# Kernel tuning notes

Hardware: AMD Instinct MI355X
Metric: run time of the kernel (lower is better)

## Reference

```python
import jax, jax.numpy as jnp
import numpy as np

DIM = 192
HEADS = 6
WS = 7
N = WS * WS  # 49
B_ = 4096
NW = 64


def _relative_position_index(ws):
    coords = np.stack(np.meshgrid(np.arange(ws), np.arange(ws), indexing='ij'))  # (2, ws, ws)
    cf = coords.reshape(2, -1)  # (2, N)
    rel = cf[:, :, None] - cf[:, None, :]  # (2, N, N)
    rel = rel.transpose(1, 2, 0).copy()
    rel[:, :, 0] += ws - 1
    rel[:, :, 1] += ws - 1
    rel[:, :, 0] *= 2 * ws - 1
    return jnp.asarray(rel.sum(-1), dtype=jnp.int32)  # (N, N)


def setup_inputs() -> dict:
    key = jax.random.key(0)
    ks = jax.random.split(key, 8)
    x = jax.random.normal(ks[0], (B_, N, DIM), dtype=jnp.float32)
    mask = jax.random.normal(ks[1], (NW, N, N), dtype=jnp.float32)
    qkv_w = jax.random.normal(ks[2], (3 * DIM, DIM), dtype=jnp.float32) * 0.02
    qkv_b = jnp.zeros((3 * DIM,), dtype=jnp.float32)
    proj_w = jax.random.normal(ks[3], (DIM, DIM), dtype=jnp.float32) * 0.02
    proj_b = jnp.zeros((DIM,), dtype=jnp.float32)
    n_bias = (2 * WS - 1) * (2 * WS - 1)  # 169
    bias_table = jax.random.truncated_normal(ks[4], -2.0, 2.0, (n_bias, HEADS), dtype=jnp.float32) * 0.02
    rel_idx = _relative_position_index(WS)
    return {"x": x, "mask": mask, "qkv_w": qkv_w, "qkv_b": qkv_b,
            "proj_w": proj_w, "proj_b": proj_b, "bias_table": bias_table,
            "rel_idx": rel_idx}


def reference(x, mask, qkv_w, qkv_b, proj_w, proj_b, bias_table, rel_idx):
    Bw, n, c = x.shape
    hd = c // HEADS
    scale = hd ** -0.5
    qkv = x @ qkv_w.T + qkv_b  # (B_, N, 3C)
    qkv = qkv.reshape(Bw, n, 3, HEADS, hd).transpose(2, 0, 3, 1, 4)  # (3, B_, H, N, hd)
    q, k, v = qkv[0] * scale, qkv[1], qkv[2]
    attn = jnp.einsum('bhqd,bhkd->bhqk', q, k)  # (B_, H, N, N)
    bias = bias_table[rel_idx.reshape(-1)].reshape(n, n, HEADS).transpose(2, 0, 1)  # (H, N, N)
    attn = attn + bias[None]
    nW = mask.shape[0]
    attn = attn.reshape(Bw // nW, nW, HEADS, n, n) + mask[None, :, None]
    attn = jax.nn.softmax(attn.reshape(Bw, HEADS, n, n), axis=-1)
    out = jnp.einsum('bhqk,bhkd->bhqd', attn, v)  # (B_, H, N, hd)
    out = out.transpose(0, 2, 1, 3).reshape(Bw, n, c)
    return out @ proj_w.T + proj_b
```

## Files before the change

### kernel.cpp

```cpp
#include <hip/hip_runtime.h>
#include <hip/hip_fp16.h>


typedef short bf16x8 __attribute__((ext_vector_type(8)));
typedef float f32x4 __attribute__((ext_vector_type(4)));

#define MFMA16(a, b, c) __builtin_amdgcn_mfma_f32_16x16x32_bf16((a), (b), (c), 0, 0, 0)

#define DIMC 192
#define NTOK 49

__device__ __forceinline__ unsigned short f2bf(float f) {
  unsigned int u = __float_as_uint(f);
  u += 0x7fffu + ((u >> 16) & 1u);
  return (unsigned short)(u >> 16);
}

__global__ void prep_kernel(const float* __restrict__ qkv_w,
                            const float* __restrict__ proj_w,
                            const float* __restrict__ bias_table,
                            const int* __restrict__ rel_idx,
                            unsigned short* __restrict__ qkv_wb,
                            unsigned short* __restrict__ proj_wb,
                            float* __restrict__ biasP) {
  int i = blockIdx.x * 256 + threadIdx.x;
  if (i < 576 * 192) qkv_wb[i] = f2bf(qkv_w[i]);
  if (i < 192 * 192) proj_wb[i] = f2bf(proj_w[i]);
  if (i < 6 * 64 * 64) {
    int h = i >> 12;
    int rr = i & 4095;
    int r = rr >> 6, c = rr & 63;
    float v = 0.f;
    if (r < NTOK && c < NTOK) v = bias_table[rel_idx[r * NTOK + c] * 6 + h];
    biasP[i] = v;
  }
}

__global__ __launch_bounds__(256, 2) void winattn_kernel(
    const float* __restrict__ x,
    const float* __restrict__ mask,
    const float* __restrict__ qkv_b,
    const float* __restrict__ proj_b,
    const unsigned short* __restrict__ qkv_wb,
    const unsigned short* __restrict__ proj_wb,
    const float* __restrict__ biasP,
    float* __restrict__ out) {
  __shared__ unsigned short xb[64 * 200];
  __shared__ unsigned short Qs[64 * 40];
  __shared__ unsigned short Ks[64 * 40];
  __shared__ unsigned short Vts[32 * 72];
  __shared__ unsigned short Pb[4 * 16 * 72];
  __shared__ unsigned short Ob[64 * 40];
  __shared__ __half maskS[64 * 64];

  const int tid = threadIdx.x;
  const int b = blockIdx.x;
  const int widx = b & 63;
  const int lane = tid & 63;
  const int wv = tid >> 6;
  const int lq = lane >> 4;
  const int ln = lane & 15;

  {
    const float4* xp = (const float4*)(x + (size_t)b * (NTOK * DIMC));
    for (int i = tid; i < NTOK * DIMC / 4; i += 256) {
      float4 v = xp[i];
      int fl = i * 4;
      int r = fl / DIMC;
      int c = fl - r * DIMC;
      unsigned int lo = (unsigned int)f2bf(v.x) | ((unsigned int)f2bf(v.y) << 16);
      unsigned int hi = (unsigned int)f2bf(v.z) | ((unsigned int)f2bf(v.w) << 16);
      *(uint2*)(&xb[r * 200 + c]) = make_uint2(lo, hi);
    }
    for (int i = tid; i < 15 * 200 / 2; i += 256)
      ((unsigned int*)(&xb[49 * 200]))[i] = 0u;
    const float* mp = mask + (size_t)widx * (NTOK * NTOK);
    for (int i = tid; i < 64 * 64; i += 256) {
      int r = i >> 6, c = i & 63;
      float v = (c >= NTOK) ? -30000.f : ((r >= NTOK) ? 0.f : mp[r * NTOK + c]);
      maskS[i] = __float2half(v);
    }
  }

  f32x4 pacc[4][3];
  for (int nti = 0; nti < 3; ++nti) {
    float pbv = proj_b[(wv * 3 + nti) * 16 + ln];
    for (int mt = 0; mt < 4; ++mt) pacc[mt][nti] = (f32x4){pbv, pbv, pbv, pbv};
  }
  __syncthreads();

  const float scale = 0.17677669529663687f;

  for (int h = 0; h < 6; ++h) {
    for (int tt = 0; tt < 6; tt += 2) {
      int t0 = wv * 6 + tt;
      int t1 = t0 + 1;
      int nt0 = t0 >> 2, mt0 = t0 & 3;
      int nt1 = t1 >> 2, mt1 = t1 & 3;
      int oc0 = (nt0 >> 1) * DIMC + h * 32 + (nt0 & 1) * 16 + ln;
      int oc1 = (nt1 >> 1) * DIMC + h * 32 + (nt1 & 1) * 16 + ln;
      const unsigned short* w0p = qkv_wb + (size_t)oc0 * DIMC + lq * 8;
      const unsigned short* w1p = qkv_wb + (size_t)oc1 * DIMC + lq * 8;
      bf16x8 w0[6], w1[6];
      for (int ks = 0; ks < 6; ++ks) {
        w0[ks] = *(const bf16x8*)(w0p + ks * 32);
        w1[ks] = *(const bf16x8*)(w1p + ks * 32);
      }
      float b0 = qkv_b[oc0], b1 = qkv_b[oc1];
      f32x4 acc0 = (f32x4){b0, b0, b0, b0};
      f32x4 acc1 = (f32x4){b1, b1, b1, b1};
      const unsigned short* a0p = &xb[(mt0 * 16 + ln) * 200 + lq * 8];
      const unsigned short* a1p = &xb[(mt1 * 16 + ln) * 200 + lq * 8];
      for (int ks = 0; ks < 6; ++ks) {
        bf16x8 a0 = *(const bf16x8*)(a0p + ks * 32);
        bf16x8 a1 = *(const bf16x8*)(a1p + ks * 32);
        acc0 = MFMA16(a0, w0[ks], acc0);
        acc1 = MFMA16(a1, w1[ks], acc1);
      }
      {
        int which = nt0 >> 1, db = (nt0 & 1) * 16 + ln, row0 = mt0 * 16 + lq * 4;
        if (which == 0) {
          for (int r = 0; r < 4; ++r) Qs[(row0 + r) * 40 + db] = f2bf(acc0[r] * scale);
        } else if (which == 1) {
          for (int r = 0; r < 4; ++r) Ks[(row0 + r) * 40 + db] = f2bf(acc0[r]);
        } else {
          unsigned int lo = (unsigned int)f2bf(acc0[0]) | ((unsigned int)f2bf(acc0[1]) << 16);
          unsigned int hi = (unsigned int)f2bf(acc0[2]) | ((unsigned int)f2bf(acc0[3]) << 16);
          *(uint2*)(&Vts[db * 72 + row0]) = make_uint2(lo, hi);
        }
      }
      {
        int which = nt1 >> 1, db = (nt1 & 1) * 16 + ln, row0 = mt1 * 16 + lq * 4;
        if (which == 0) {
          for (int r = 0; r < 4; ++r) Qs[(row0 + r) * 40 + db] = f2bf(acc1[r] * scale);
        } else if (which == 1) {
          for (int r = 0; r < 4; ++r) Ks[(row0 + r) * 40 + db] = f2bf(acc1[r]);
        } else {
          unsigned int lo = (unsigned int)f2bf(acc1[0]) | ((unsigned int)f2bf(acc1[1]) << 16);
          unsigned int hi = (unsigned int)f2bf(acc1[2]) | ((unsigned int)f2bf(acc1[3]) << 16);
          *(uint2*)(&Vts[db * 72 + row0]) = make_uint2(lo, hi);
        }
      }
    }
    __syncthreads();

    {
      const int mt = wv;
      bf16x8 kf[4], vf0[2], vf1[2];
      for (int nt = 0; nt < 4; ++nt)
        kf[nt] = *(const bf16x8*)&Ks[(nt * 16 + ln) * 40 + lq * 8];
      for (int nv = 0; nv < 2; ++nv) {
        vf0[nv] = *(const bf16x8*)&Vts[(nv * 16 + ln) * 72 + lq * 8];
        vf1[nv] = *(const bf16x8*)&Vts[(nv * 16 + ln) * 72 + 32 + lq * 8];
      }
      bf16x8 qf = *(const bf16x8*)&Qs[(mt * 16 + ln) * 40 + lq * 8];
      f32x4 sv[4];
      for (int nt = 0; nt < 4; ++nt)
        sv[nt] = MFMA16(qf, kf[nt], ((f32x4){0.f, 0.f, 0.f, 0.f}));

      int row0 = mt * 16 + lq * 4;
      const float* bp = biasP + ((size_t)h * 64 + row0) * 64;
      float tt[4][4];
      for (int nt = 0; nt < 4; ++nt) {
        int col = nt * 16 + ln;
        for (int r = 0; r < 4; ++r)
          tt[nt][r] = sv[nt][r] + bp[r * 64 + col] + __half2float(maskS[(row0 + r) * 64 + col]);
      }
      float pinv[4];
      for (int r = 0; r < 4; ++r) {
        float m = fmaxf(fmaxf(tt[0][r], tt[1][r]), fmaxf(tt[2][r], tt[3][r]));
        m = fmaxf(m, __shfl_xor(m, 1, 64));
        m = fmaxf(m, __shfl_xor(m, 2, 64));
        m = fmaxf(m, __shfl_xor(m, 4, 64));
        m = fmaxf(m, __shfl_xor(m, 8, 64));
        float sum = 0.f;
        for (int nt = 0; nt < 4; ++nt) {
          float e = __expf(tt[nt][r] - m);
          tt[nt][r] = e;
          sum += e;
        }
        sum += __shfl_xor(sum, 1, 64);
        sum += __shfl_xor(sum, 2, 64);
        sum += __shfl_xor(sum, 4, 64);
        sum += __shfl_xor(sum, 8, 64);
        pinv[r] = 1.f / sum;
      }
      unsigned short* Pw = &Pb[wv * 16 * 72];
      for (int nt = 0; nt < 4; ++nt) {
        int col = nt * 16 + ln;
        for (int r = 0; r < 4; ++r) Pw[(lq * 4 + r) * 72 + col] = f2bf(tt[nt][r]);
      }
      bf16x8 pa0 = *(const bf16x8*)&Pw[ln * 72 + lq * 8];
      bf16x8 pa1 = *(const bf16x8*)&Pw[ln * 72 + 32 + lq * 8];
      f32x4 o0 = (f32x4){0.f, 0.f, 0.f, 0.f};
      f32x4 o1 = (f32x4){0.f, 0.f, 0.f, 0.f};
      o0 = MFMA16(pa0, vf0[0], o0);
      o0 = MFMA16(pa1, vf1[0], o0);
      o1 = MFMA16(pa0, vf0[1], o1);
      o1 = MFMA16(pa1, vf1[1], o1);
      for (int r = 0; r < 4; ++r) {
        int row = row0 + r;
        Ob[row * 40 + ln] = f2bf(o0[r] * pinv[r]);
        Ob[row * 40 + 16 + ln] = f2bf(o1[r] * pinv[r]);
      }
    }
    __syncthreads();

    {
      bf16x8 oa[4];
      for (int mt = 0; mt < 4; ++mt)
        oa[mt] = *(const bf16x8*)&Ob[(mt * 16 + ln) * 40 + lq * 8];
      for (int nti = 0; nti < 3; ++nti) {
        int o = (wv * 3 + nti) * 16 + ln;
        bf16x8 w = *(const bf16x8*)(proj_wb + (size_t)o * DIMC + h * 32 + lq * 8);
        for (int mt = 0; mt < 4; ++mt)
          pacc[mt][nti] = MFMA16(oa[mt], w, pacc[mt][nti]);
      }
    }
    __syncthreads();
  }

  {
    float* outp = out + (size_t)b * (NTOK * DIMC);
    for (int nti = 0; nti < 3; ++nti) {
      int col = (wv * 3 + nti) * 16 + ln;
      for (int mt = 0; mt < 4; ++mt) {
        int row0 = mt * 16 + lq * 4;
        for (int r = 0; r < 4; ++r) {
          int row = row0 + r;
          if (row < NTOK) outp[row * DIMC + col] = pacc[mt][nti][r];
        }
      }
    }
  }
}

extern "C" void kernel_launch(void* const* d_in, const int* in_sizes, int n_in,
                              void* d_out, int out_size, void* d_ws, size_t ws_size,
                              hipStream_t stream) {
  const float* x = (const float*)d_in[0];
  const float* mask = (const float*)d_in[1];
  const float* qkv_w = (const float*)d_in[2];
  const float* qkv_b = (const float*)d_in[3];
  const float* proj_w = (const float*)d_in[4];
  const float* proj_b = (const float*)d_in[5];
  const float* bias_table = (const float*)d_in[6];
  const int* rel_idx = (const int*)d_in[7];

  unsigned short* qkv_wb = (unsigned short*)d_ws;
  unsigned short* proj_wb = qkv_wb + 576 * 192;
  float* biasP = (float*)(proj_wb + 192 * 192);

  prep_kernel<<<432, 256, 0, stream>>>(qkv_w, proj_w, bias_table, rel_idx,
                                       qkv_wb, proj_wb, biasP);
  winattn_kernel<<<4096, 256, 0, stream>>>(x, mask, qkv_b, proj_b,
                                           qkv_wb, proj_wb, biasP,
                                           (float*)d_out);
}
```

Before: 611.6 us.

## Alias shared buffers, keep mask in registers, raise occupancy to four blocks

Shared memory drops from about 63KB to about 40KB. The separate buffers become one array with phase-aliased regions: P scratch overlays Q/K, and Ob overlays K/V, made safe by an extra barrier after the fragments are loaded. The per-window mask tile is now loaded directly into registers instead of a half-precision LDS copy. Launch bounds are raised to 4 blocks per CU, and the QKV projection loop is simplified to one tile per iteration with full unrolling. The aim is higher occupancy to hide latency, at the cost of an extra barrier per head and a tighter register budget that may cause spills.

```diff
diff --git a/kernel.cpp b/kernel.cpp
--- a/kernel.cpp
+++ b/kernel.cpp
@@ -36,7 +36,7 @@
   }
 }
 
-__global__ __launch_bounds__(256, 2) void winattn_kernel(
+__global__ __launch_bounds__(256, 4) void winattn_kernel(
     const float* __restrict__ x,
     const float* __restrict__ mask,
     const float* __restrict__ qkv_b,
@@ -45,13 +45,12 @@
     const unsigned short* __restrict__ proj_wb,
     const float* __restrict__ biasP,
     float* __restrict__ out) {
-  __shared__ unsigned short xb[64 * 200];
-  __shared__ unsigned short Qs[64 * 40];
-  __shared__ unsigned short Ks[64 * 40];
-  __shared__ unsigned short Vts[32 * 72];
-  __shared__ unsigned short Pb[4 * 16 * 72];
-  __shared__ unsigned short Ob[64 * 40];
-  __shared__ __half maskS[64 * 64];
+  __shared__ unsigned short smem[20224];
+  unsigned short* xb = smem;
+  unsigned short* Qs = smem + 12800;
+  unsigned short* Ks = smem + 15360;
+  unsigned short* Vts = smem + 17920;
+  unsigned short* Ob = smem + 17408;
 
   const int tid = threadIdx.x;
   const int b = blockIdx.x;
@@ -61,30 +60,43 @@
   const int lq = lane >> 4;
   const int ln = lane & 15;
 
+  unsigned short* Pbw = smem + 12800 + wv * (16 * 72);
+
   {
     const float4* xp = (const float4*)(x + (size_t)b * (NTOK * DIMC));
     for (int i = tid; i < NTOK * DIMC / 4; i += 256) {
       float4 v = xp[i];
-      int fl = i * 4;
-      int r = fl / DIMC;
-      int c = fl - r * DIMC;
+      int r = i / 48;
+      int c = (i - r * 48) * 4;
       unsigned int lo = (unsigned int)f2bf(v.x) | ((unsigned int)f2bf(v.y) << 16);
       unsigned int hi = (unsigned int)f2bf(v.z) | ((unsigned int)f2bf(v.w) << 16);
       *(uint2*)(&xb[r * 200 + c]) = make_uint2(lo, hi);
     }
     for (int i = tid; i < 15 * 200 / 2; i += 256)
       ((unsigned int*)(&xb[49 * 200]))[i] = 0u;
+  }
+
+  const int arow0 = wv * 16 + lq * 4;
+  float mk[4][4];
+  {
     const float* mp = mask + (size_t)widx * (NTOK * NTOK);
-    for (int i = tid; i < 64 * 64; i += 256) {
-      int r = i >> 6, c = i & 63;
-      float v = (c >= NTOK) ? -30000.f : ((r >= NTOK) ? 0.f : mp[r * NTOK + c]);
-      maskS[i] = __float2half(v);
+#pragma unroll
+    for (int nt = 0; nt < 4; ++nt) {
+      int col = nt * 16 + ln;
+#pragma unroll
+      for (int r = 0; r < 4; ++r) {
+        int row = arow0 + r;
+        mk[nt][r] = (col >= NTOK) ? -30000.f
+                                  : ((row >= NTOK) ? 0.f : mp[row * NTOK + col]);
+      }
     }
   }
 
   f32x4 pacc[4][3];
+#pragma unroll
   for (int nti = 0; nti < 3; ++nti) {
     float pbv = proj_b[(wv * 3 + nti) * 16 + ln];
+#pragma unroll
     for (int mt = 0; mt < 4; ++mt) pacc[mt][nti] = (f32x4){pbv, pbv, pbv, pbv};
   }
   __syncthreads();
@@ -92,81 +104,67 @@
   const float scale = 0.17677669529663687f;
 
   for (int h = 0; h < 6; ++h) {
-    for (int tt = 0; tt < 6; tt += 2) {
-      int t0 = wv * 6 + tt;
-      int t1 = t0 + 1;
-      int nt0 = t0 >> 2, mt0 = t0 & 3;
-      int nt1 = t1 >> 2, mt1 = t1 & 3;
-      int oc0 = (nt0 >> 1) * DIMC + h * 32 + (nt0 & 1) * 16 + ln;
-      int oc1 = (nt1 >> 1) * DIMC + h * 32 + (nt1 & 1) * 16 + ln;
-      const unsigned short* w0p = qkv_wb + (size_t)oc0 * DIMC + lq * 8;
-      const unsigned short* w1p = qkv_wb + (size_t)oc1 * DIMC + lq * 8;
-      bf16x8 w0[6], w1[6];
+#pragma unroll
+    for (int t = 0; t < 6; ++t) {
+      int id = wv * 6 + t;
+      int nt = id >> 2, mt = id & 3;
+      int oc = (nt >> 1) * DIMC + h * 32 + (nt & 1) * 16 + ln;
+      const unsigned short* wp = qkv_wb + (size_t)oc * DIMC + lq * 8;
+      bf16x8 w[6];
+#pragma unroll
+      for (int ks = 0; ks < 6; ++ks) w[ks] = *(const bf16x8*)(wp + ks * 32);
+      float b0 = qkv_b[oc];
+      f32x4 acc = (f32x4){b0, b0, b0, b0};
+      const unsigned short* ap = &xb[(mt * 16 + ln) * 200 + lq * 8];
+#pragma unroll
       for (int ks = 0; ks < 6; ++ks) {
-        w0[ks] = *(const bf16x8*)(w0p + ks * 32);
-        w1[ks] = *(const bf16x8*)(w1p + ks * 32);
-      }
-      float b0 = qkv_b[oc0], b1 = qkv_b[oc1];
-      f32x4 acc0 = (f32x4){b0, b0, b0, b0};
-      f32x4 acc1 = (f32x4){b1, b1, b1, b1};
-      const unsigned short* a0p = &xb[(mt0 * 16 + ln) * 200 + lq * 8];
-      const unsigned short* a1p = &xb[(mt1 * 16 + ln) * 200 + lq * 8];
-      for (int ks = 0; ks < 6; ++ks) {
-        bf16x8 a0 = *(const bf16x8*)(a0p + ks * 32);
-        bf16x8 a1 = *(const bf16x8*)(a1p + ks * 32);
-        acc0 = MFMA16(a0, w0[ks], acc0);
-        acc1 = MFMA16(a1, w1[ks], acc1);
-      }
-      {
-        int which = nt0 >> 1, db = (nt0 & 1) * 16 + ln, row0 = mt0 * 16 + lq * 4;
-        if (which == 0) {
-          for (int r = 0; r < 4; ++r) Qs[(row0 + r) * 40 + db] = f2bf(acc0[r] * scale);
-        } else if (which == 1) {
-          for (int r = 0; r < 4; ++r) Ks[(row0 + r) * 40 + db] = f2bf(acc0[r]);
-        } else {
-          unsigned int lo = (unsigned int)f2bf(acc0[0]) | ((unsigned int)f2bf(acc0[1]) << 16);
-          unsigned int hi = (unsigned int)f2bf(acc0[2]) | ((unsigned int)f2bf(acc0[3]) << 16);
-          *(uint2*)(&Vts[db * 72 + row0]) = make_uint2(lo, hi);
-        }
-      }
-      {
-        int which = nt1 >> 1, db = (nt1 & 1) * 16 + ln, row0 = mt1 * 16 + lq * 4;
-        if (which == 0) {
-          for (int r = 0; r < 4; ++r) Qs[(row0 + r) * 40 + db] = f2bf(acc1[r] * scale);
-        } else if (which == 1) {
-          for (int r = 0; r < 4; ++r) Ks[(row0 + r) * 40 + db] = f2bf(acc1[r]);
-        } else {
-          unsigned int lo = (unsigned int)f2bf(acc1[0]) | ((unsigned int)f2bf(acc1[1]) << 16);
-          unsigned int hi = (unsigned int)f2bf(acc1[2]) | ((unsigned int)f2bf(acc1[3]) << 16);
-          *(uint2*)(&Vts[db * 72 + row0]) = make_uint2(lo, hi);
-        }
+        bf16x8 a = *(const bf16x8*)(ap + ks * 32);
+        acc = MFMA16(a, w[ks], acc);
+      }
+      int which = nt >> 1, db = (nt & 1) * 16 + ln, row0 = mt * 16 + lq * 4;
+      if (which == 0) {
+#pragma unroll
+        for (int r = 0; r < 4; ++r) Qs[(row0 + r) * 40 + db] = f2bf(acc[r] * scale);
+      } else if (which == 1) {
+#pragma unroll
+        for (int r = 0; r < 4; ++r) Ks[(row0 + r) * 40 + db] = f2bf(acc[r]);
+      } else {
+        unsigned int lo = (unsigned int)f2bf(acc[0]) | ((unsigned int)f2bf(acc[1]) << 16);
+        unsigned int hi = (unsigned int)f2bf(acc[2]) | ((unsigned int)f2bf(acc[3]) << 16);
+        *(uint2*)(&Vts[db * 72 + row0]) = make_uint2(lo, hi);
       }
     }
     __syncthreads();
 
     {
-      const int mt = wv;
       bf16x8 kf[4], vf0[2], vf1[2];
+#pragma unroll
       for (int nt = 0; nt < 4; ++nt)
         kf[nt] = *(const bf16x8*)&Ks[(nt * 16 + ln) * 40 + lq * 8];
+#pragma unroll
       for (int nv = 0; nv < 2; ++nv) {
         vf0[nv] = *(const bf16x8*)&Vts[(nv * 16 + ln) * 72 + lq * 8];
         vf1[nv] = *(const bf16x8*)&Vts[(nv * 16 + ln) * 72 + 32 + lq * 8];
       }
-      bf16x8 qf = *(const bf16x8*)&Qs[(mt * 16 + ln) * 40 + lq * 8];
+      bf16x8 qf = *(const bf16x8*)&Qs[(wv * 16 + ln) * 40 + lq * 8];
+      __syncthreads();
+
       f32x4 sv[4];
+#pragma unroll
       for (int nt = 0; nt < 4; ++nt)
         sv[nt] = MFMA16(qf, kf[nt], ((f32x4){0.f, 0.f, 0.f, 0.f}));
 
-      int row0 = mt * 16 + lq * 4;
-      const float* bp = biasP + ((size_t)h * 64 + row0) * 64;
+      const float* bp = biasP + ((size_t)h * 64 + arow0) * 64;
       float tt[4][4];
+#pragma unroll
       for (int nt = 0; nt < 4; ++nt) {
         int col = nt * 16 + ln;
+#pragma unroll
         for (int r = 0; r < 4; ++r)
-          tt[nt][r] = sv[nt][r] + bp[r * 64 + col] + __half2float(maskS[(row0 + r) * 64 + col]);
+          tt[nt][r] = sv[nt][r] + bp[r * 64 + col] + mk[nt][r];
       }
       float pinv[4];
+#pragma unroll
       for (int r = 0; r < 4; ++r) {
         float m = fmaxf(fmaxf(tt[0][r], tt[1][r]), fmaxf(tt[2][r], tt[3][r]));
         m = fmaxf(m, __shfl_xor(m, 1, 64));
@@ -174,6 +172,7 @@
         m = fmaxf(m, __shfl_xor(m, 4, 64));
         m = fmaxf(m, __shfl_xor(m, 8, 64));
         float sum = 0.f;
+#pragma unroll
         for (int nt = 0; nt < 4; ++nt) {
           float e = __expf(tt[nt][r] - m);
           tt[nt][r] = e;
@@ -185,21 +184,23 @@
         sum += __shfl_xor(sum, 8, 64);
         pinv[r] = 1.f / sum;
       }
-      unsigned short* Pw = &Pb[wv * 16 * 72];
+#pragma unroll
       for (int nt = 0; nt < 4; ++nt) {
         int col = nt * 16 + ln;
-        for (int r = 0; r < 4; ++r) Pw[(lq * 4 + r) * 72 + col] = f2bf(tt[nt][r]);
-      }
-      bf16x8 pa0 = *(const bf16x8*)&Pw[ln * 72 + lq * 8];
-      bf16x8 pa1 = *(const bf16x8*)&Pw[ln * 72 + 32 + lq * 8];
+#pragma unroll
+        for (int r = 0; r < 4; ++r) Pbw[(lq * 4 + r) * 72 + col] = f2bf(tt[nt][r]);
+      }
+      bf16x8 pa0 = *(const bf16x8*)&Pbw[ln * 72 + lq * 8];
+      bf16x8 pa1 = *(const bf16x8*)&Pbw[ln * 72 + 32 + lq * 8];
       f32x4 o0 = (f32x4){0.f, 0.f, 0.f, 0.f};
       f32x4 o1 = (f32x4){0.f, 0.f, 0.f, 0.f};
       o0 = MFMA16(pa0, vf0[0], o0);
       o0 = MFMA16(pa1, vf1[0], o0);
       o1 = MFMA16(pa0, vf0[1], o1);
       o1 = MFMA16(pa1, vf1[1], o1);
+#pragma unroll
       for (int r = 0; r < 4; ++r) {
-        int row = row0 + r;
+        int row = arow0 + r;
         Ob[row * 40 + ln] = f2bf(o0[r] * pinv[r]);
         Ob[row * 40 + 16 + ln] = f2bf(o1[r] * pinv[r]);
       }
@@ -208,11 +209,14 @@
 
     {
       bf16x8 oa[4];
+#pragma unroll
       for (int mt = 0; mt < 4; ++mt)
         oa[mt] = *(const bf16x8*)&Ob[(mt * 16 + ln) * 40 + lq * 8];
+#pragma unroll
       for (int nti = 0; nti < 3; ++nti) {
         int o = (wv * 3 + nti) * 16 + ln;
         bf16x8 w = *(const bf16x8*)(proj_wb + (size_t)o * DIMC + h * 32 + lq * 8);
+#pragma unroll
         for (int mt = 0; mt < 4; ++mt)
           pacc[mt][nti] = MFMA16(oa[mt], w, pacc[mt][nti]);
       }
@@ -222,10 +226,13 @@
 
   {
     float* outp = out + (size_t)b * (NTOK * DIMC);
+#pragma unroll
     for (int nti = 0; nti < 3; ++nti) {
       int col = (wv * 3 + nti) * 16 + ln;
+#pragma unroll
       for (int mt = 0; mt < 4; ++mt) {
         int row0 = mt * 16 + lq * 4;
+#pragma unroll
         for (int r = 0; r < 4; ++r) {
           int row = row0 + r;
           if (row < NTOK) outp[row * DIMC + col] = pacc[mt][nti][r];
```

New measurement: 851.0 us. +39.1%, slower.
